# Kernel optimization log

Hardware: AMD Instinct MI355X
Metric: run time of the kernel (lower is better)

Reference implementation:

```python
import jax, jax.numpy as jnp
import numpy as np

DIM = 2048
DIM_HEADS = 64
NUM_HEADS = DIM // DIM_HEADS  # 32


def setup_inputs() -> dict:
    key = jax.random.key(0)
    k1, k2, k3, k4 = jax.random.split(key, 4)
    B, N = 2, 2048
    x = jax.random.normal(k1, (B, N, DIM), dtype=jnp.float32)
    freqs = jax.random.normal(k2, (N, DIM_HEADS), dtype=jnp.float32)
    W_qkv = jax.random.normal(k3, (3 * DIM, DIM), dtype=jnp.float32) * 0.02
    W_out = jax.random.normal(k4, (DIM, DIM), dtype=jnp.float32) * 0.02
    return {"x": x, "freqs": freqs, "W_qkv": W_qkv, "W_out": W_out}


def _rotate_half(x):
    # split last dim into two halves (j=2), return cat(-x2, x1)
    x1, x2 = jnp.split(x, 2, axis=-1)
    return jnp.concatenate([-x2, x1], axis=-1)


def _apply_rotary_pos_emb(t, freqs, scale=1.0):
    # t: [b, h, n, d]; freqs: [n, rot_dim]; rotary math in float32
    out_dtype = t.dtype
    rot_dim = freqs.shape[-1]
    seq_len = t.shape[-2]
    freqs = freqs.astype(jnp.float32)[-seq_len:, :]  # [n, rot_dim]
    t = t.astype(jnp.float32)
    t_rot, t_unrot = t[..., :rot_dim], t[..., rot_dim:]
    t_rot = t_rot * jnp.cos(freqs) * scale + _rotate_half(t_rot) * jnp.sin(freqs) * scale
    return jnp.concatenate([t_rot.astype(out_dtype), t_unrot.astype(out_dtype)], axis=-1)


def reference(x, freqs, W_qkv, W_out):
    B, N, _ = x.shape
    h, d = NUM_HEADS, DIM_HEADS
    # fused QKV projection (Linear, no bias): x @ W_qkv.T
    qkv = jnp.einsum('bnc,fc->bnf', x, W_qkv)  # [B, N, 3*DIM]
    q, k, v = jnp.split(qkv, 3, axis=-1)
    q = q.reshape(B, N, h, d).transpose(0, 2, 1, 3)  # [B, h, N, d]
    k = k.reshape(B, N, h, d).transpose(0, 2, 1, 3)
    v = v.reshape(B, N, h, d).transpose(0, 2, 1, 3)
    # equal q/k seq lens -> ratio = 1, same freqs for both
    q = _apply_rotary_pos_emb(q, freqs)
    k = _apply_rotary_pos_emb(k, freqs)
    # scaled dot-product attention (non-causal)
    scale = 1.0 / np.sqrt(d).astype(np.float32)
    scores = jnp.einsum('bhqd,bhkd->bhqk', q, k) * scale
    attn = jax.nn.softmax(scores, axis=-1)
    out = jnp.einsum('bhqk,bhkd->bhqd', attn, v)
    out = out.transpose(0, 2, 1, 3).reshape(B, N, h * d)  # [B, N, DIM]
    return jnp.einsum('bnc,oc->bno', out, W_out)
```

## Files before the change

### kernel.cpp

```cpp
#include <hip/hip_runtime.h>

#define DIMC 2048
#define NSEQ 2048
#define NBATCH 2
#define NH 32
#define DH 64
#define BHEADS (NBATCH*NH)
#define MROWS (NBATCH*NSEQ)
#define NQKV (3*DIMC)

typedef __attribute__((ext_vector_type(8))) short short8;
typedef __attribute__((ext_vector_type(4))) float f32x4;
typedef __attribute__((ext_vector_type(4))) unsigned int uint4v;
typedef __attribute__((ext_vector_type(2))) unsigned int u32x2;

static __device__ __forceinline__ unsigned short f2bf(float f) {
  union { float f; unsigned int u; } v; v.f = f;
  unsigned int r = (v.u + 0x7FFFu + ((v.u >> 16) & 1u)) >> 16;
  return (unsigned short)r;
}

static __device__ __forceinline__ unsigned int cvt_pk_bf16(float lo, float hi) {
  unsigned int r;
  asm("v_cvt_pk_bf16_f32 %0, %1, %2" : "=v"(r) : "v"(lo), "v"(hi));
  return r;
}

__global__ __launch_bounds__(256) void cvt_bf16(const float* __restrict__ in,
                                                unsigned short* __restrict__ out,
                                                int n8) {
  int i = blockIdx.x * blockDim.x + threadIdx.x;
  int stride = gridDim.x * blockDim.x;
  for (; i < n8; i += stride) {
    const float4* p = (const float4*)in + (size_t)i * 2;
    float4 a = p[0], b = p[1];
    union { unsigned short u[8]; uint4v v; } o;
    o.u[0] = f2bf(a.x); o.u[1] = f2bf(a.y); o.u[2] = f2bf(a.z); o.u[3] = f2bf(a.w);
    o.u[4] = f2bf(b.x); o.u[5] = f2bf(b.y); o.u[6] = f2bf(b.z); o.u[7] = f2bf(b.w);
    *((uint4v*)out + i) = o.v;
  }
}

__global__ __launch_bounds__(256) void build_cs(const float* __restrict__ freqs,
                                                float2* __restrict__ cs, int n) {
  int i = blockIdx.x * blockDim.x + threadIdx.x;
  if (i < n) { float f = freqs[i]; cs[i] = make_float2(cosf(f), sinf(f)); }
}

#define QSCALE 0.18033688011112042f

template<int EPI>
__global__ __launch_bounds__(256) void gemm_bt(
    const unsigned short* __restrict__ A,
    const unsigned short* __restrict__ Bm,
    int Kdim, int Ncols,
    float* __restrict__ Cout,
    unsigned short* __restrict__ qo, unsigned short* __restrict__ ko,
    unsigned short* __restrict__ vo, const float2* __restrict__ cs)
{
  __shared__ __align__(16) unsigned short Al[128 * 32];
  __shared__ __align__(16) unsigned short Bl[128 * 32];
  const int t = threadIdx.x;
  const int w = t >> 6, lane = t & 63, lr = lane & 15, g = lane >> 4;
  const int m0 = blockIdx.y * 128;
  const int n0 = blockIdx.x * 128;
  const int wm = w >> 1, wn = w & 1;
  const int xs = (lr & 3) ^ ((lr >> 2) & 3);

  f32x4 acc[4][4];
  f32x4 zero = {0.0f, 0.0f, 0.0f, 0.0f};
  #pragma unroll
  for (int i = 0; i < 4; i++)
    #pragma unroll
    for (int j = 0; j < 4; j++) acc[i][j] = zero;

  int roww[2], swo[2];
  #pragma unroll
  for (int c = 0; c < 2; c++) {
    int off = c * 4096 + t * 16;
    int row = off >> 6;
    int col16 = (off >> 4) & 3;
    int sw = col16 ^ ((row & 3) ^ ((row >> 2) & 3));
    roww[c] = row; swo[c] = sw * 8;
  }

  for (int k0 = 0; k0 < Kdim; k0 += 32) {
    #pragma unroll
    for (int c = 0; c < 2; c++) {
      const unsigned short* sa = A  + (size_t)(m0 + roww[c]) * Kdim + k0 + swo[c];
      const unsigned short* sb = Bm + (size_t)(n0 + roww[c]) * Kdim + k0 + swo[c];
      __builtin_amdgcn_global_load_lds(
          (const __attribute__((address_space(1))) void*)sa,
          (__attribute__((address_space(3))) void*)(Al + c * 2048 + w * 512), 16, 0, 0);
      __builtin_amdgcn_global_load_lds(
          (const __attribute__((address_space(1))) void*)sb,
          (__attribute__((address_space(3))) void*)(Bl + c * 2048 + w * 512), 16, 0, 0);
    }
    __syncthreads();

    short8 af[4], bfr[4];
    #pragma unroll
    for (int m = 0; m < 4; m++) {
      int row = wm * 64 + m * 16 + lr;
      af[m] = *(const short8*)&Al[row * 32 + (g ^ xs) * 8];
    }
    #pragma unroll
    for (int n = 0; n < 4; n++) {
      int row = wn * 64 + n * 16 + lr;
      bfr[n] = *(const short8*)&Bl[row * 32 + (g ^ xs) * 8];
    }
    #pragma unroll
    for (int m = 0; m < 4; m++)
      #pragma unroll
      for (int n = 0; n < 4; n++)
        acc[m][n] = __builtin_amdgcn_mfma_f32_16x16x32_bf16(af[m], bfr[n], acc[m][n], 0, 0, 0);
    __syncthreads();
  }

  if (EPI == 0) {
    #pragma unroll
    for (int m = 0; m < 4; m++) {
      #pragma unroll
      for (int r = 0; r < 4; r++) {
        int row = m0 + wm * 64 + m * 16 + g * 4 + r;
        #pragma unroll
        for (int n = 0; n < 4; n++) {
          int col = n0 + wn * 64 + n * 16 + lr;
          Cout[(size_t)row * Ncols + col] = acc[m][n][r];
        }
      }
    }
  } else {
    const int which = n0 >> 11;
    const int colbase = (n0 + wn * 64) & 2047;
    const int head = colbase >> 6;
    #pragma unroll
    for (int m = 0; m < 4; m++) {
      #pragma unroll
      for (int r = 0; r < 4; r++) {
        int row = m0 + wm * 64 + m * 16 + g * 4 + r;
        int b = row >> 11, ntok = row & 2047;
        size_t obase = ((size_t)(b * NH + head) * NSEQ + ntok) * DH;
        #pragma unroll
        for (int n = 0; n < 4; n++) {
          int d = n * 16 + lr;
          float val = acc[m][n][r];
          if (which == 2) {
            vo[obase + d] = f2bf(val);
          } else {
            float other = acc[m][n ^ 2][r];
            float2 c2 = cs[ntok * DH + d];
            float rot = (d < 32) ? (val * c2.x - other * c2.y)
                                 : (val * c2.x + other * c2.y);
            if (which == 0) qo[obase + d] = f2bf(rot * QSCALE);
            else            ko[obase + d] = f2bf(rot);
          }
        }
      }
    }
  }
}

__global__ __launch_bounds__(256, 4) void attn_fa(
    const unsigned short* __restrict__ qb,
    const unsigned short* __restrict__ kb,
    const unsigned short* __restrict__ vb,
    unsigned short* __restrict__ aob)
{
  __shared__ __align__(16) unsigned short Kl[64 * 64];
  __shared__ __align__(16) unsigned short Vt[64 * 72];
  __shared__ __align__(16) unsigned short Pl[4][32 * 72];

  const int t = threadIdx.x;
  const int w = t >> 6, lane = t & 63, lr = lane & 15, g = lane >> 4;
  const int bh = blockIdx.y;
  const int q0 = blockIdx.x * 128 + w * 32;
  const size_t hbase = (size_t)bh * NSEQ * DH;

  short8 qf[2][2];
  #pragma unroll
  for (int qt = 0; qt < 2; qt++)
    #pragma unroll
    for (int hf = 0; hf < 2; hf++)
      qf[qt][hf] = *(const short8*)(qb + hbase + (size_t)(q0 + qt * 16 + lr) * DH + hf * 32 + g * 8);

  f32x4 zero = {0.0f, 0.0f, 0.0f, 0.0f};
  f32x4 oacc[2][4];
  #pragma unroll
  for (int qt = 0; qt < 2; qt++)
    #pragma unroll
    for (int dv = 0; dv < 4; dv++) oacc[qt][dv] = zero;
  float mrun[2] = {-1e30f, -1e30f};
  float lrun[2] = {0.0f, 0.0f};

  int kro[2], kdo_[2];
  #pragma unroll
  for (int c = 0; c < 2; c++) {
    int b = w * 2048 + c * 1024 + lane * 16;
    int row = b >> 7;
    int off = b ^ ((row & 7) << 4);
    kro[c] = row;
    kdo_[c] = (off >> 1) & 63;
  }
  const int vr0 = (t & 31) * 2;
  const int vhv = (t >> 5) * 8;

  unsigned short* prow0 = &Pl[w][lr * 72];
  unsigned short* prow1 = &Pl[w][(16 + lr) * 72];

  for (int kv0 = 0; kv0 < NSEQ; kv0 += 64) {
    __syncthreads();
    #pragma unroll
    for (int c = 0; c < 2; c++) {
      const unsigned short* src = kb + hbase + (size_t)(kv0 + kro[c]) * DH + kdo_[c];
      __builtin_amdgcn_global_load_lds(
          (const __attribute__((address_space(1))) void*)src,
          (__attribute__((address_space(3))) void*)(Kl + w * 1024 + c * 512), 16, 0, 0);
    }
    {
      const unsigned short* s0 = vb + hbase + (size_t)(kv0 + vr0) * DH + vhv;
      short8 v0 = *(const short8*)(s0);
      short8 v1 = *(const short8*)(s0 + DH);
      #pragma unroll
      for (int j = 0; j < 8; j++) {
        unsigned int p = ((unsigned short)v0[j]) | (((unsigned int)(unsigned short)v1[j]) << 16);
        *(unsigned int*)&Vt[(vhv + j) * 72 + vr0] = p;
      }
    }
    __syncthreads();

    f32x4 s[2][4];
    #pragma unroll
    for (int kt = 0; kt < 4; kt++) {
      int row = kt * 16 + lr;
      int sw = (row & 7) << 4;
      int byteA = (row * 128 + g * 16) ^ sw;
      int byteB = (row * 128 + 64 + g * 16) ^ sw;
      short8 kA = *(const short8*)((const char*)Kl + byteA);
      short8 kB = *(const short8*)((const char*)Kl + byteB);
      #pragma unroll
      for (int qt = 0; qt < 2; qt++) {
        f32x4 a0 = __builtin_amdgcn_mfma_f32_16x16x32_bf16(kA, qf[qt][0], zero, 0, 0, 0);
        s[qt][kt] = __builtin_amdgcn_mfma_f32_16x16x32_bf16(kB, qf[qt][1], a0, 0, 0, 0);
      }
    }

    float nm[2];
    #pragma unroll
    for (int qt = 0; qt < 2; qt++) {
      f32x4 m01 = s[qt][0];
      #pragma unroll
      for (int kt = 1; kt < 4; kt++) {
        f32x4 sv = s[qt][kt];
        m01[0] = fmaxf(m01[0], sv[0]); m01[1] = fmaxf(m01[1], sv[1]);
        m01[2] = fmaxf(m01[2], sv[2]); m01[3] = fmaxf(m01[3], sv[3]);
      }
      float v = fmaxf(fmaxf(m01[0], m01[1]), fmaxf(m01[2], m01[3]));
      v = fmaxf(v, __shfl_xor(v, 16));
      v = fmaxf(v, __shfl_xor(v, 32));
      nm[qt] = v;
    }

    if (!__all(fmaxf(nm[0] - mrun[0], nm[1] - mrun[1]) <= 8.0f)) {
      const int sb = (lane & 48) + ((lane & 48) >> 2);
      #pragma unroll
      for (int qt = 0; qt < 2; qt++) {
        float m2 = fmaxf(mrun[qt], nm[qt]);
        float cc = exp2f(mrun[qt] - m2);
        mrun[qt] = m2;
        lrun[qt] *= cc;
        float c0r = __shfl(cc, sb + 0);
        float c1r = __shfl(cc, sb + 1);
        float c2r = __shfl(cc, sb + 2);
        float c3r = __shfl(cc, sb + 3);
        #pragma unroll
        for (int dv = 0; dv < 4; dv++) {
          f32x4 a = oacc[qt][dv];
          a[0] *= c0r; a[1] *= c1r; a[2] *= c2r; a[3] *= c3r;
          oacc[qt][dv] = a;
        }
      }
    }

    #pragma unroll
    for (int qt = 0; qt < 2; qt++) {
      float mq = mrun[qt];
      float ls = 0.0f;
      unsigned short* prow = qt ? prow1 : prow0;
      #pragma unroll
      for (int kt = 0; kt < 4; kt++) {
        f32x4 sv = s[qt][kt];
        float p0 = exp2f(sv[0] - mq), p1 = exp2f(sv[1] - mq);
        float p2 = exp2f(sv[2] - mq), p3 = exp2f(sv[3] - mq);
        ls += (p0 + p1) + (p2 + p3);
        u32x2 uu;
        uu.x = cvt_pk_bf16(p0, p1);
        uu.y = cvt_pk_bf16(p2, p3);
        *(u32x2*)(prow + kt * 16 + g * 4) = uu;
      }
      ls += __shfl_xor(ls, 16);
      ls += __shfl_xor(ls, 32);
      lrun[qt] += ls;
    }

    #pragma unroll
    for (int c0 = 0; c0 < 2; c0++) {
      short8 pa0 = *(const short8*)(prow0 + c0 * 32 + g * 8);
      short8 pa1 = *(const short8*)(prow1 + c0 * 32 + g * 8);
      #pragma unroll
      for (int dv = 0; dv < 4; dv++) {
        short8 vf = *(const short8*)&Vt[(dv * 16 + lr) * 72 + c0 * 32 + g * 8];
        oacc[0][dv] = __builtin_amdgcn_mfma_f32_16x16x32_bf16(pa0, vf, oacc[0][dv], 0, 0, 0);
        oacc[1][dv] = __builtin_amdgcn_mfma_f32_16x16x32_bf16(pa1, vf, oacc[1][dv], 0, 0, 0);
      }
    }
  }

  const int b = bh >> 5, h = bh & 31;
  const int sb = (lane & 48) + ((lane & 48) >> 2);
  #pragma unroll
  for (int qt = 0; qt < 2; qt++) {
    float inv = 1.0f / lrun[qt];
    float ir[4];
    ir[0] = __shfl(inv, sb + 0);
    ir[1] = __shfl(inv, sb + 1);
    ir[2] = __shfl(inv, sb + 2);
    ir[3] = __shfl(inv, sb + 3);
    #pragma unroll
    for (int r = 0; r < 4; r++) {
      int ntok = q0 + qt * 16 + g * 4 + r;
      size_t ob = ((size_t)(b * NSEQ + ntok)) * DIMC + h * DH;
      #pragma unroll
      for (int dv = 0; dv < 4; dv++)
        aob[ob + dv * 16 + lr] = f2bf(oacc[qt][dv][r] * ir[r]);
    }
  }
}

extern "C" void kernel_launch(void* const* d_in, const int* in_sizes, int n_in,
                              void* d_out, int out_size, void* d_ws, size_t ws_size,
                              hipStream_t stream) {
  const float* x     = (const float*)d_in[0];
  const float* freqs = (const float*)d_in[1];
  const float* Wqkv  = (const float*)d_in[2];
  const float* Wout  = (const float*)d_in[3];
  float* out = (float*)d_out;

  char* ws = (char*)d_ws;
  size_t off = 0;
  auto alloc = [&](size_t bytes) {
    void* p = ws + off;
    off += (bytes + 255) & ~(size_t)255;
    return p;
  };
  unsigned short* xb    = (unsigned short*)alloc((size_t)MROWS * DIMC * 2);
  unsigned short* wqkvb = (unsigned short*)alloc((size_t)NQKV * DIMC * 2);
  unsigned short* woutb = (unsigned short*)alloc((size_t)DIMC * DIMC * 2);
  unsigned short* qbuf  = (unsigned short*)alloc((size_t)BHEADS * NSEQ * DH * 2);
  unsigned short* kbuf  = (unsigned short*)alloc((size_t)BHEADS * NSEQ * DH * 2);
  unsigned short* vbuf  = (unsigned short*)alloc((size_t)BHEADS * NSEQ * DH * 2);
  float2* cst           = (float2*)alloc((size_t)NSEQ * DH * sizeof(float2));
  unsigned short* aob   = xb;

  cvt_bf16<<<2048, 256, 0, stream>>>(x, xb, MROWS * DIMC / 8);
  cvt_bf16<<<2048, 256, 0, stream>>>(Wqkv, wqkvb, NQKV * DIMC / 8);
  cvt_bf16<<<1024, 256, 0, stream>>>(Wout, woutb, DIMC * DIMC / 8);
  build_cs<<<(NSEQ * DH + 255) / 256, 256, 0, stream>>>(freqs, cst, NSEQ * DH);

  gemm_bt<1><<<dim3(NQKV / 128, MROWS / 128), 256, 0, stream>>>(
      xb, wqkvb, DIMC, NQKV, nullptr, qbuf, kbuf, vbuf, cst);

  attn_fa<<<dim3(NSEQ / 128, BHEADS), 256, 0, stream>>>(qbuf, kbuf, vbuf, aob);

  gemm_bt<0><<<dim3(DIMC / 128, MROWS / 128), 256, 0, stream>>>(
      aob, woutb, DIMC, DIMC, out, nullptr, nullptr, nullptr, nullptr);
}
```

Measured before the change: 376.7 us.

## Replace 128x128 GEMM with 256x256 double-buffered ping-pong MFMA kernel

```diff
diff --git a/kernel.cpp b/kernel.cpp
--- a/kernel.cpp
+++ b/kernel.cpp
@@ -25,6 +25,11 @@
   asm("v_cvt_pk_bf16_f32 %0, %1, %2" : "=v"(r) : "v"(lo), "v"(hi));
   return r;
 }
+
+#define BAR()    __builtin_amdgcn_s_barrier()
+#define LGKM0()  asm volatile("s_waitcnt lgkmcnt(0)" ::: "memory")
+#define LGKM8()  asm volatile("s_waitcnt lgkmcnt(8)" ::: "memory")
+#define VM(n)    asm volatile("s_waitcnt vmcnt(" #n ")" ::: "memory")
 
 __global__ __launch_bounds__(256) void cvt_bf16(const float* __restrict__ in,
                                                 unsigned short* __restrict__ out,
@@ -50,7 +55,7 @@
 #define QSCALE 0.18033688011112042f
 
 template<int EPI>
-__global__ __launch_bounds__(256) void gemm_bt(
+__global__ __launch_bounds__(512, 2) void gemm256(
     const unsigned short* __restrict__ A,
     const unsigned short* __restrict__ Bm,
     int Kdim, int Ncols,
@@ -58,87 +63,146 @@
     unsigned short* __restrict__ qo, unsigned short* __restrict__ ko,
     unsigned short* __restrict__ vo, const float2* __restrict__ cs)
 {
-  __shared__ __align__(16) unsigned short Al[128 * 32];
-  __shared__ __align__(16) unsigned short Bl[128 * 32];
+  extern __shared__ char Lds[];
   const int t = threadIdx.x;
   const int w = t >> 6, lane = t & 63, lr = lane & 15, g = lane >> 4;
-  const int m0 = blockIdx.y * 128;
-  const int n0 = blockIdx.x * 128;
-  const int wm = w >> 1, wn = w & 1;
-  const int xs = (lr & 3) ^ ((lr >> 2) & 3);
-
-  f32x4 acc[4][4];
+  const int wm = w >> 2, wn = w & 3;
+  const int gx = (g * 16) ^ ((lr & 4) << 3);
+
+  const int nx = gridDim.x;
+  int orig = blockIdx.y * nx + blockIdx.x;
+  int cpx = (nx * gridDim.y) >> 3;
+  int id = (orig & 7) * cpx + (orig >> 3);
+  const int m0 = (id / nx) * 256;
+  const int n0 = (id % nx) * 256;
+
+  const int lp = lane ^ ((lane & 32) >> 4);
+  const unsigned short* sbase[2][2][2];
+  #pragma unroll
+  for (int c = 0; c < 2; c++) {
+    int srow = w * 16 + c * 8 + (lp >> 3);
+    int scol = (lp & 7) * 8;
+    sbase[0][0][c] = A  + (size_t)(m0 + srow) * Kdim + scol;
+    sbase[0][1][c] = A  + (size_t)(m0 + 128 + srow) * Kdim + scol;
+    sbase[1][0][c] = Bm + (size_t)(n0 + srow) * Kdim + scol;
+    sbase[1][1][c] = Bm + (size_t)(n0 + 128 + srow) * Kdim + scol;
+  }
+
+  auto STAGE = [&](int op, int half, int buf, int T) {
+    const unsigned short* s0 = sbase[op][half][0] + (size_t)T * 64;
+    const unsigned short* s1 = sbase[op][half][1] + (size_t)T * 64;
+    char* d = Lds + buf * 65536 + op * 32768 + half * 16384 + w * 2048;
+    __builtin_amdgcn_global_load_lds(
+        (const __attribute__((address_space(1))) void*)s0,
+        (__attribute__((address_space(3))) void*)d, 16, 0, 0);
+    __builtin_amdgcn_global_load_lds(
+        (const __attribute__((address_space(1))) void*)s1,
+        (__attribute__((address_space(3))) void*)(d + 1024), 16, 0, 0);
+  };
+
+  short8 A0r[2][4], A1r[2][4], B0r[2][2], B1r[2][2];
+
+  auto LDA = [&](short8 (&dst)[2][4], int bufb, int mlo) {
+    const char* bp = Lds + bufb + wm * 16384 + (mlo * 16 + lr) * 128 + gx;
+    #pragma unroll
+    for (int ks = 0; ks < 2; ks++)
+      #pragma unroll
+      for (int mm = 0; mm < 4; mm++)
+        dst[ks][mm] = *(const short8*)(bp + mm * 2048 + ks * 64);
+  };
+  auto LDB = [&](short8 (&dst)[2][2], int bufb, int nlo) {
+    const char* bp = Lds + bufb + 32768 + (wn >> 1) * 16384 + (wn & 1) * 8192
+                     + (nlo * 16 + lr) * 128 + gx;
+    #pragma unroll
+    for (int ks = 0; ks < 2; ks++)
+      #pragma unroll
+      for (int nn = 0; nn < 2; nn++)
+        dst[ks][nn] = *(const short8*)(bp + nn * 2048 + ks * 64);
+  };
+
+  f32x4 acc[8][4];
   f32x4 zero = {0.0f, 0.0f, 0.0f, 0.0f};
   #pragma unroll
-  for (int i = 0; i < 4; i++)
+  for (int i = 0; i < 8; i++)
     #pragma unroll
     for (int j = 0; j < 4; j++) acc[i][j] = zero;
 
-  int roww[2], swo[2];
-  #pragma unroll
-  for (int c = 0; c < 2; c++) {
-    int off = c * 4096 + t * 16;
-    int row = off >> 6;
-    int col16 = (off >> 4) & 3;
-    int sw = col16 ^ ((row & 3) ^ ((row >> 2) & 3));
-    roww[c] = row; swo[c] = sw * 8;
-  }
-
-  for (int k0 = 0; k0 < Kdim; k0 += 32) {
-    #pragma unroll
-    for (int c = 0; c < 2; c++) {
-      const unsigned short* sa = A  + (size_t)(m0 + roww[c]) * Kdim + k0 + swo[c];
-      const unsigned short* sb = Bm + (size_t)(n0 + roww[c]) * Kdim + k0 + swo[c];
-      __builtin_amdgcn_global_load_lds(
-          (const __attribute__((address_space(1))) void*)sa,
-          (__attribute__((address_space(3))) void*)(Al + c * 2048 + w * 512), 16, 0, 0);
-      __builtin_amdgcn_global_load_lds(
-          (const __attribute__((address_space(1))) void*)sb,
-          (__attribute__((address_space(3))) void*)(Bl + c * 2048 + w * 512), 16, 0, 0);
-    }
-    __syncthreads();
-
-    short8 af[4], bfr[4];
-    #pragma unroll
-    for (int m = 0; m < 4; m++) {
-      int row = wm * 64 + m * 16 + lr;
-      af[m] = *(const short8*)&Al[row * 32 + (g ^ xs) * 8];
-    }
-    #pragma unroll
-    for (int n = 0; n < 4; n++) {
-      int row = wn * 64 + n * 16 + lr;
-      bfr[n] = *(const short8*)&Bl[row * 32 + (g ^ xs) * 8];
-    }
-    #pragma unroll
-    for (int m = 0; m < 4; m++)
-      #pragma unroll
-      for (int n = 0; n < 4; n++)
-        acc[m][n] = __builtin_amdgcn_mfma_f32_16x16x32_bf16(af[m], bfr[n], acc[m][n], 0, 0, 0);
-    __syncthreads();
+  auto MM = [&](short8 (&Af)[2][4], short8 (&Bf)[2][2], int mq, int nq) {
+    __builtin_amdgcn_s_setprio(1);
+    #pragma unroll
+    for (int mm = 0; mm < 4; mm++)
+      #pragma unroll
+      for (int nn = 0; nn < 2; nn++)
+        #pragma unroll
+        for (int ks = 0; ks < 2; ks++)
+          acc[mq * 4 + mm][nq * 2 + nn] = __builtin_amdgcn_mfma_f32_16x16x32_bf16(
+              Af[ks][mm], Bf[ks][nn], acc[mq * 4 + mm][nq * 2 + nn], 0, 0, 0);
+    __builtin_amdgcn_s_setprio(0);
+  };
+
+  STAGE(0,0,0, 0); STAGE(1,0,0, 0); STAGE(0,1,0, 0); STAGE(1,1,0, 0);
+  STAGE(0,0,1, 1); STAGE(1,0,1, 1); STAGE(0,1,1, 1);
+  VM(6);
+  BAR();
+  LDA(A0r, 0, 0); LDB(B0r, 0, 0);
+
+  const int NIT = Kdim >> 7;
+  for (int i = 0; i < NIT; i++) {
+    const bool more = (i < NIT - 1);
+    const int Tc  = 2 * i + 1;
+    const int Tn0 = 2 * i + 2;
+    const int Tn1 = 2 * i + 3;
+    LDA(A1r, 0, 4);
+    STAGE(1,1,1, Tc);
+    BAR(); LGKM0(); MM(A0r, B0r, 0, 0); BAR();
+    LDB(B1r, 0, 2);
+    if (more) STAGE(0,0,0, Tn0);
+    BAR(); LGKM0(); MM(A1r, B0r, 1, 0); BAR();
+    if (more) STAGE(1,0,0, Tn0);
+    BAR(); LGKM0(); MM(A1r, B1r, 1, 1);
+    if (more) { VM(4); } else { VM(0); }
+    BAR();
+    LDA(A1r, 65536, 0); LDB(B0r, 65536, 0);
+    if (more) STAGE(0,1,0, Tn0);
+    LGKM8();
+    BAR(); LGKM0(); MM(A0r, B1r, 0, 1); BAR();
+    LDA(A0r, 65536, 4);
+    if (more) STAGE(1,1,0, Tn0);
+    BAR(); LGKM0(); MM(A1r, B0r, 0, 0); BAR();
+    LDB(B1r, 65536, 2);
+    if (more) STAGE(0,0,1, Tn1);
+    BAR(); LGKM0(); MM(A0r, B0r, 1, 0); BAR();
+    if (more) STAGE(1,0,1, Tn1);
+    BAR(); LGKM0(); MM(A0r, B1r, 1, 1);
+    if (more) VM(4);
+    BAR();
+    if (more) {
+      LDA(A0r, 0, 0); LDB(B0r, 0, 0);
+      STAGE(0,1,1, Tn1);
+      LGKM8();
+    }
+    BAR(); LGKM0(); MM(A1r, B1r, 0, 1); BAR();
   }
 
   if (EPI == 0) {
     #pragma unroll
-    for (int m = 0; m < 4; m++) {
+    for (int m = 0; m < 8; m++) {
       #pragma unroll
       for (int r = 0; r < 4; r++) {
-        int row = m0 + wm * 64 + m * 16 + g * 4 + r;
+        int row = m0 + wm * 128 + m * 16 + g * 4 + r;
         #pragma unroll
-        for (int n = 0; n < 4; n++) {
-          int col = n0 + wn * 64 + n * 16 + lr;
-          Cout[(size_t)row * Ncols + col] = acc[m][n][r];
-        }
+        for (int n = 0; n < 4; n++)
+          Cout[(size_t)row * Ncols + (n0 + wn * 64 + n * 16 + lr)] = acc[m][n][r];
       }
     }
   } else {
     const int which = n0 >> 11;
-    const int colbase = (n0 + wn * 64) & 2047;
-    const int head = colbase >> 6;
-    #pragma unroll
-    for (int m = 0; m < 4; m++) {
+    const int head = ((n0 & 2047) + wn * 64) >> 6;
+    #pragma unroll
+    for (int m = 0; m < 8; m++) {
       #pragma unroll
       for (int r = 0; r < 4; r++) {
-        int row = m0 + wm * 64 + m * 16 + g * 4 + r;
+        int row = m0 + wm * 128 + m * 16 + g * 4 + r;
         int b = row >> 11, ntok = row & 2047;
         size_t obase = ((size_t)(b * NH + head) * NSEQ + ntok) * DH;
         #pragma unroll
@@ -362,16 +426,21 @@
   float2* cst           = (float2*)alloc((size_t)NSEQ * DH * sizeof(float2));
   unsigned short* aob   = xb;
 
+  (void)hipFuncSetAttribute((const void*)gemm256<1>,
+      hipFuncAttributeMaxDynamicSharedMemorySize, 131072);
+  (void)hipFuncSetAttribute((const void*)gemm256<0>,
+      hipFuncAttributeMaxDynamicSharedMemorySize, 131072);
+
   cvt_bf16<<<2048, 256, 0, stream>>>(x, xb, MROWS * DIMC / 8);
   cvt_bf16<<<2048, 256, 0, stream>>>(Wqkv, wqkvb, NQKV * DIMC / 8);
   cvt_bf16<<<1024, 256, 0, stream>>>(Wout, woutb, DIMC * DIMC / 8);
   build_cs<<<(NSEQ * DH + 255) / 256, 256, 0, stream>>>(freqs, cst, NSEQ * DH);
 
-  gemm_bt<1><<<dim3(NQKV / 128, MROWS / 128), 256, 0, stream>>>(
+  gemm256<1><<<dim3(NQKV / 256, MROWS / 256), 512, 131072, stream>>>(
       xb, wqkvb, DIMC, NQKV, nullptr, qbuf, kbuf, vbuf, cst);
 
   attn_fa<<<dim3(NSEQ / 128, BHEADS), 256, 0, stream>>>(qbuf, kbuf, vbuf, aob);
 
-  gemm_bt<0><<<dim3(DIMC / 128, MROWS / 128), 256, 0, stream>>>(
+  gemm256<0><<<dim3(DIMC / 256, MROWS / 256), 512, 131072, stream>>>(
       aob, woutb, DIMC, DIMC, out, nullptr, nullptr, nullptr, nullptr);
 }
```

Measured after the change: 505.5 us. 1.34x slower.

## Rewrite projection GEMMs as triple-buffered 128x256 tiles with 512 threads

Applied to the files above, without the earlier changes.

```diff
diff --git a/kernel.cpp b/kernel.cpp
--- a/kernel.cpp
+++ b/kernel.cpp
@@ -25,6 +25,11 @@
   asm("v_cvt_pk_bf16_f32 %0, %1, %2" : "=v"(r) : "v"(lo), "v"(hi));
   return r;
 }
+
+#define BAR()    __builtin_amdgcn_s_barrier()
+#define FENCE()  asm volatile("" ::: "memory")
+#define LGKM0()  asm volatile("s_waitcnt lgkmcnt(0)" ::: "memory")
+#define VM(n)    asm volatile("s_waitcnt vmcnt(" #n ")" ::: "memory")
 
 __global__ __launch_bounds__(256) void cvt_bf16(const float* __restrict__ in,
                                                 unsigned short* __restrict__ out,
@@ -48,9 +53,10 @@
 }
 
 #define QSCALE 0.18033688011112042f
+#define SLOT 24576
 
 template<int EPI>
-__global__ __launch_bounds__(256) void gemm_bt(
+__global__ __launch_bounds__(512, 1) void gemm128(
     const unsigned short* __restrict__ A,
     const unsigned short* __restrict__ Bm,
     int Kdim, int Ncols,
@@ -58,14 +64,46 @@
     unsigned short* __restrict__ qo, unsigned short* __restrict__ ko,
     unsigned short* __restrict__ vo, const float2* __restrict__ cs)
 {
-  __shared__ __align__(16) unsigned short Al[128 * 32];
-  __shared__ __align__(16) unsigned short Bl[128 * 32];
+  extern __shared__ char Lds[];
   const int t = threadIdx.x;
   const int w = t >> 6, lane = t & 63, lr = lane & 15, g = lane >> 4;
-  const int m0 = blockIdx.y * 128;
-  const int n0 = blockIdx.x * 128;
-  const int wm = w >> 1, wn = w & 1;
-  const int xs = (lr & 3) ^ ((lr >> 2) & 3);
+  const int wm = w >> 2, wn = w & 3;
+
+  const int nx = gridDim.x;
+  int orig = blockIdx.y * nx + blockIdx.x;
+  int cpx = (nx * gridDim.y) >> 3;
+  int id = (orig & 7) * cpx + (orig >> 3);
+  const int m0 = (id / nx) * 128;
+  const int n0 = (id % nx) * 256;
+
+  const int rowt = t >> 2, colt = (t & 3) * 8;
+  const unsigned short* Abase = A + (size_t)(m0 + rowt) * Kdim + colt;
+  const unsigned short* Bbase = Bm + (size_t)(n0 + rowt) * Kdim + colt;
+  char* dstw = Lds + w * 1024;
+
+  auto STAGE = [&](int sbuf, int T) {
+    const unsigned short* sa = Abase + T * 32;
+    const unsigned short* sb = Bbase + T * 32;
+    __builtin_amdgcn_global_load_lds(
+        (const __attribute__((address_space(1))) void*)sa,
+        (__attribute__((address_space(3))) void*)(dstw + sbuf), 16, 0, 0);
+    __builtin_amdgcn_global_load_lds(
+        (const __attribute__((address_space(1))) void*)sb,
+        (__attribute__((address_space(3))) void*)(dstw + sbuf + 8192), 16, 0, 0);
+    __builtin_amdgcn_global_load_lds(
+        (const __attribute__((address_space(1))) void*)(sb + (size_t)128 * Kdim),
+        (__attribute__((address_space(3))) void*)(dstw + sbuf + 16384), 16, 0, 0);
+  };
+
+  short8 Af[4], Bf[4];
+  auto LDAB = [&](int rb) {
+    const char* ap = Lds + rb + (wm * 64 + lr) * 64 + g * 16;
+    const char* bp = Lds + rb + 8192 + (wn * 64 + lr) * 64 + g * 16;
+    #pragma unroll
+    for (int m = 0; m < 4; m++) Af[m] = *(const short8*)(ap + m * 1024);
+    #pragma unroll
+    for (int n = 0; n < 4; n++) Bf[n] = *(const short8*)(bp + n * 1024);
+  };
 
   f32x4 acc[4][4];
   f32x4 zero = {0.0f, 0.0f, 0.0f, 0.0f};
@@ -74,47 +112,27 @@
     #pragma unroll
     for (int j = 0; j < 4; j++) acc[i][j] = zero;
 
-  int roww[2], swo[2];
-  #pragma unroll
-  for (int c = 0; c < 2; c++) {
-    int off = c * 4096 + t * 16;
-    int row = off >> 6;
-    int col16 = (off >> 4) & 3;
-    int sw = col16 ^ ((row & 3) ^ ((row >> 2) & 3));
-    roww[c] = row; swo[c] = sw * 8;
-  }
-
-  for (int k0 = 0; k0 < Kdim; k0 += 32) {
-    #pragma unroll
-    for (int c = 0; c < 2; c++) {
-      const unsigned short* sa = A  + (size_t)(m0 + roww[c]) * Kdim + k0 + swo[c];
-      const unsigned short* sb = Bm + (size_t)(n0 + roww[c]) * Kdim + k0 + swo[c];
-      __builtin_amdgcn_global_load_lds(
-          (const __attribute__((address_space(1))) void*)sa,
-          (__attribute__((address_space(3))) void*)(Al + c * 2048 + w * 512), 16, 0, 0);
-      __builtin_amdgcn_global_load_lds(
-          (const __attribute__((address_space(1))) void*)sb,
-          (__attribute__((address_space(3))) void*)(Bl + c * 2048 + w * 512), 16, 0, 0);
-    }
-    __syncthreads();
-
-    short8 af[4], bfr[4];
-    #pragma unroll
-    for (int m = 0; m < 4; m++) {
-      int row = wm * 64 + m * 16 + lr;
-      af[m] = *(const short8*)&Al[row * 32 + (g ^ xs) * 8];
-    }
-    #pragma unroll
-    for (int n = 0; n < 4; n++) {
-      int row = wn * 64 + n * 16 + lr;
-      bfr[n] = *(const short8*)&Bl[row * 32 + (g ^ xs) * 8];
-    }
+  STAGE(0, 0); STAGE(SLOT, 1);
+  VM(3);
+  BAR(); FENCE();
+
+  const int NT = Kdim >> 5;
+  int rb = 0, sb = 2 * SLOT;
+  for (int i = 0; i < NT; i++) {
+    LDAB(rb);
+    if (i + 2 < NT) STAGE(sb, i + 2);
+    BAR(); LGKM0();
+    __builtin_amdgcn_s_setprio(1);
     #pragma unroll
     for (int m = 0; m < 4; m++)
       #pragma unroll
       for (int n = 0; n < 4; n++)
-        acc[m][n] = __builtin_amdgcn_mfma_f32_16x16x32_bf16(af[m], bfr[n], acc[m][n], 0, 0, 0);
-    __syncthreads();
+        acc[m][n] = __builtin_amdgcn_mfma_f32_16x16x32_bf16(Af[m], Bf[n], acc[m][n], 0, 0, 0);
+    __builtin_amdgcn_s_setprio(0);
+    if (i < NT - 2) { VM(3); } else { VM(0); }
+    BAR(); FENCE();
+    rb += SLOT; if (rb == 3 * SLOT) rb = 0;
+    sb += SLOT; if (sb == 3 * SLOT) sb = 0;
   }
 
   if (EPI == 0) {
@@ -124,16 +142,13 @@
       for (int r = 0; r < 4; r++) {
         int row = m0 + wm * 64 + m * 16 + g * 4 + r;
         #pragma unroll
-        for (int n = 0; n < 4; n++) {
-          int col = n0 + wn * 64 + n * 16 + lr;
-          Cout[(size_t)row * Ncols + col] = acc[m][n][r];
-        }
+        for (int n = 0; n < 4; n++)
+          Cout[(size_t)row * Ncols + (n0 + wn * 64 + n * 16 + lr)] = acc[m][n][r];
       }
     }
   } else {
     const int which = n0 >> 11;
-    const int colbase = (n0 + wn * 64) & 2047;
-    const int head = colbase >> 6;
+    const int head = ((n0 & 2047) + wn * 64) >> 6;
     #pragma unroll
     for (int m = 0; m < 4; m++) {
       #pragma unroll
@@ -362,16 +377,21 @@
   float2* cst           = (float2*)alloc((size_t)NSEQ * DH * sizeof(float2));
   unsigned short* aob   = xb;
 
+  (void)hipFuncSetAttribute((const void*)gemm128<1>,
+      hipFuncAttributeMaxDynamicSharedMemorySize, 3 * SLOT);
+  (void)hipFuncSetAttribute((const void*)gemm128<0>,
+      hipFuncAttributeMaxDynamicSharedMemorySize, 3 * SLOT);
+
   cvt_bf16<<<2048, 256, 0, stream>>>(x, xb, MROWS * DIMC / 8);
   cvt_bf16<<<2048, 256, 0, stream>>>(Wqkv, wqkvb, NQKV * DIMC / 8);
   cvt_bf16<<<1024, 256, 0, stream>>>(Wout, woutb, DIMC * DIMC / 8);
   build_cs<<<(NSEQ * DH + 255) / 256, 256, 0, stream>>>(freqs, cst, NSEQ * DH);
 
-  gemm_bt<1><<<dim3(NQKV / 128, MROWS / 128), 256, 0, stream>>>(
+  gemm128<1><<<dim3(NQKV / 256, MROWS / 128), 512, 3 * SLOT, stream>>>(
       xb, wqkvb, DIMC, NQKV, nullptr, qbuf, kbuf, vbuf, cst);
 
   attn_fa<<<dim3(NSEQ / 128, BHEADS), 256, 0, stream>>>(qbuf, kbuf, vbuf, aob);
 
-  gemm_bt<0><<<dim3(DIMC / 128, MROWS / 128), 256, 0, stream>>>(
+  gemm128<0><<<dim3(DIMC / 256, MROWS / 128), 512, 3 * SLOT, stream>>>(
       aob, woutb, DIMC, DIMC, out, nullptr, nullptr, nullptr, nullptr);
 }
```

After: 339.1 us. 10.0% less time.
